# Optimization experiments

Measured on AMD Instinct MI355X. Metric: run time of the kernel, lower is better.

Reference implementation:

```python
import jax, jax.numpy as jnp
import numpy as np

CHEB_K = 3

def avwgcn(x, E, w_pool, b_pool):
    # x: [B,N,C], E: [N,D], w_pool: [D,K,C,O], b_pool: [D,O]
    N = E.shape[0]
    supports = jax.nn.softmax(jax.nn.relu(E @ E.T), axis=1)  # [N,N]
    slist = [jnp.eye(N, dtype=x.dtype), supports]
    for _ in range(CHEB_K - 2):
        slist.append(2.0 * supports @ slist[-1] - slist[-2])
    S = jnp.stack(slist)                         # [K,N,N]
    W = jnp.einsum('nd,dkio->nkio', E, w_pool)   # [N,K,C,O]
    b = E @ b_pool                               # [N,O]
    xg = jnp.einsum('knm,bmc->bnkc', S, x)       # [B,N,K,C]
    return jnp.einsum('bnki,nkio->bno', xg, W) + b


def setup_inputs() -> dict:
    key = jax.random.key(0)
    ks = jax.random.split(key, 9)
    B, N, C_IN, C_OUT, D = 16, 2048, 64, 64, 10
    x = jax.random.normal(ks[0], (B, N, C_IN), dtype=jnp.float32)
    state = jax.random.normal(ks[1], (B, N, C_OUT), dtype=jnp.float32)
    node_embeddings = jax.random.normal(ks[2], (N, D), dtype=jnp.float32)
    gate_wpool = jax.random.normal(ks[3], (D, CHEB_K, C_IN + C_OUT, 2 * C_OUT), dtype=jnp.float32) * 0.1
    gate_bpool = jax.random.normal(ks[4], (D, 2 * C_OUT), dtype=jnp.float32) * 0.1
    upd_wpool = jax.random.normal(ks[5], (D, CHEB_K, C_IN + C_OUT, C_OUT), dtype=jnp.float32) * 0.1
    upd_bpool = jax.random.normal(ks[6], (D, C_OUT), dtype=jnp.float32) * 0.1
    lin_w = jax.random.normal(ks[7], (64, 128), dtype=jnp.float32) * 0.1
    lin_b = jax.random.normal(ks[8], (64,), dtype=jnp.float32) * 0.1
    return {"x": x, "state": state, "node_embeddings": node_embeddings,
            "gate_wpool": gate_wpool, "gate_bpool": gate_bpool,
            "upd_wpool": upd_wpool, "upd_bpool": upd_bpool,
            "lin_w": lin_w, "lin_b": lin_b}


def reference(x, state, node_embeddings, gate_wpool, gate_bpool, upd_wpool, upd_bpool, lin_w, lin_b):
    input_and_state = jnp.concatenate([x, state], axis=-1)          # [B,N,128]
    z_r = jax.nn.sigmoid(avwgcn(input_and_state, node_embeddings, gate_wpool, gate_bpool))  # [B,N,128]
    z_r = z_r @ lin_w.T + lin_b                                     # [B,N,64]
    candidate = jnp.concatenate([x, z_r], axis=-1)                  # [B,N,128]
    hc = jnp.tanh(avwgcn(candidate, node_embeddings, upd_wpool, upd_bpool))  # [B,N,64]
    return hc
```

## Files before the change

### kernel.cpp

```cpp
#include <hip/hip_runtime.h>

typedef unsigned short u16;
typedef short s16x8 __attribute__((ext_vector_type(8)));
typedef _Float16 h16x8 __attribute__((ext_vector_type(8)));
typedef float f32x4 __attribute__((ext_vector_type(4)));
typedef u16 u16x4 __attribute__((ext_vector_type(4)));

#define DEV static __device__ __forceinline__

DEV u16 f2h(float x){ union { _Float16 h; u16 u; } v; v.h = (_Float16)x; return v.u; }
DEV float h2f(u16 u){ union { u16 u; _Float16 h; } v; v.u = u; return (float)v.h; }
DEV void split_h(float x, u16& h, u16& l){
    h = f2h(x);
    l = f2h(x - h2f(h));
}
DEV h16x8 H8(s16x8 v){ union { s16x8 s; h16x8 h; } u; u.s = v; return u.h; }
DEV f32x4 mfma16(s16x8 a, s16x8 b, f32x4 c){
    return __builtin_amdgcn_mfma_f32_16x16x32_f16(H8(a), H8(b), c, 0, 0, 0);
}

DEV int swz(int r, int m){ return (m & ~0x38) | ((((m >> 3) ^ r) & 7) << 3); }

DEV void gll16(const u16* g, u16* l){
    __builtin_amdgcn_global_load_lds((const __attribute__((address_space(1))) void*)g,
                                     (__attribute__((address_space(3))) void*)l, 16, 0, 0);
}

__global__ __launch_bounds__(256) void k_prep(const float* __restrict__ E,
    const float* __restrict__ gwp, const float* __restrict__ gbp,
    const float* __restrict__ uwp, const float* __restrict__ ubp,
    const float* __restrict__ lw,
    u16* __restrict__ wg, u16* __restrict__ wu,
    float* __restrict__ bg, float* __restrict__ bu,
    u16* __restrict__ lwt,
    u16* __restrict__ Sh, u16* __restrict__ Sl)
{
    __shared__ float red[8];
    const int tid = threadIdx.x;
    if (blockIdx.x < 2048){
        const int n = blockIdx.x;
        const int w = tid >> 6, lane = tid & 63;
        float en[10];
        #pragma unroll
        for (int d = 0; d < 10; d++) en[d] = E[n*10 + d];
        float v[8];
        #pragma unroll
        for (int i = 0; i < 8; i++){
            int m = tid + i*256;
            const float* em = E + m*10;
            float s = 0.f;
            #pragma unroll
            for (int d = 0; d < 10; d++) s += en[d]*em[d];
            v[i] = fmaxf(s, 0.f);
        }
        float mx = v[0];
        #pragma unroll
        for (int i = 1; i < 8; i++) mx = fmaxf(mx, v[i]);
        #pragma unroll
        for (int off = 32; off > 0; off >>= 1) mx = fmaxf(mx, __shfl_xor(mx, off));
        if (lane == 0) red[w] = mx;
        __syncthreads();
        mx = fmaxf(fmaxf(red[0], red[1]), fmaxf(red[2], red[3]));
        __syncthreads();
        float sum = 0.f;
        #pragma unroll
        for (int i = 0; i < 8; i++){ v[i] = __expf(v[i] - mx); sum += v[i]; }
        #pragma unroll
        for (int off = 32; off > 0; off >>= 1) sum += __shfl_xor(sum, off);
        if (lane == 0) red[4 + w] = sum;
        __syncthreads();
        sum = red[4] + red[5] + red[6] + red[7];
        float inv = 1.f / sum;
        #pragma unroll
        for (int i = 0; i < 8; i++){
            float p = v[i] * inv;
            u16 h, l; split_h(p, h, l);
            int ms = swz(n, tid + i*256);
            Sh[n*2048 + ms] = h;
            Sl[n*2048 + ms] = l;
        }
        return;
    }
    long idx = (long)(blockIdx.x - 2048)*256 + tid;
    if (idx < 491520){
        int kk = (int)(idx & 31);
        int o  = (int)((idx >> 5) & 127);
        int r2 = (int)(idx >> 12);
        int d = r2 % 10, jc = r2 / 10;
        int j = jc*32 + kk;
        int k = j >> 7, i = j & 127;
        float v = gwp[(((d*3 + k)*128) + i)*128 + o];
        wg[idx] = f2h(v);
    } else if (idx < 737280){
        long t = idx - 491520;
        int kk = (int)(t & 31);
        int o  = (int)((t >> 5) & 63);
        int r2 = (int)(t >> 11);
        int d = r2 % 10, jc = r2 / 10;
        int j = jc*32 + kk;
        int k = j >> 7, i = j & 127;
        float v = uwp[(((d*3 + k)*128) + i)*64 + o];
        wu[t] = f2h(v);
    } else if (idx < 999424){
        long t = idx - 737280; int n = (int)(t >> 7), o = (int)(t & 127);
        float s = 0.f;
        #pragma unroll
        for (int d = 0; d < 10; d++) s += E[n*10+d]*gbp[d*128+o];
        bg[t] = s;
    } else if (idx < 1130496){
        long t = idx - 999424; int n = (int)(t >> 6), o = (int)(t & 63);
        float s = 0.f;
        #pragma unroll
        for (int d = 0; d < 10; d++) s += E[n*10+d]*ubp[d*64+o];
        bu[t] = s;
    } else if (idx < 1138688){
        long t = idx - 1130496;
        lwt[t] = f2h(lw[t]);
    }
}

__global__ __launch_bounds__(256) void k_packx(const float* __restrict__ x,
                                               const float* __restrict__ state,
                                               u16* __restrict__ xt)
{
    __shared__ u16 T[64*264];
    const int tid = threadIdx.x;
    const int ct = blockIdx.x & 31;
    const int mt = blockIdx.x >> 5;
    const int colG0 = ct << 6;
    const int m0 = mt << 8;
    const int b = colG0 >> 7, c0 = colG0 & 127;
    const float* src = (c0 < 64) ? (x + ((long)b*2048 + m0)*64)
                                 : (state + ((long)b*2048 + m0)*64);
    #pragma unroll
    for (int p = 0; p < 16; p++){
        int m = p*16 + (tid >> 4);
        int c4 = (tid & 15) << 2;
        f32x4 v = *(const f32x4*)(src + (long)m*64 + c4);
        #pragma unroll
        for (int q = 0; q < 4; q++)
            T[(c4 + q)*264 + m] = f2h(v[q]);
    }
    __syncthreads();
    #pragma unroll
    for (int p = 0; p < 8; p++){
        int cg = (tid >> 5) + p*8;
        int colG = colG0 + cg;
        int mc = (tid & 31) << 3;
        s16x8 val = *(const s16x8*)&T[cg*264 + mc];
        int ms = swz(colG, m0 + mc);
        *(s16x8*)(xt + (long)colG*2048 + ms) = val;
    }
}

template<int EPI>
__global__ __launch_bounds__(256) void k_gemm(
    const u16* __restrict__ Ah, const u16* __restrict__ Al,
    const u16* __restrict__ Bt,
    u16* __restrict__ Ot, float* __restrict__ Orow,
    const u16* __restrict__ Xt)
{
    __shared__ __attribute__((aligned(16))) u16 AsH[2][64*64];
    __shared__ __attribute__((aligned(16))) u16 AsL[2][64*64];
    __shared__ __attribute__((aligned(16))) u16 Bs[2][128*64];
    const int tid = threadIdx.x;
    const int xc = blockIdx.x & 7, ii = blockIdx.x >> 3;
    const int bm = ((xc & 3)*8 + (ii & 7)) << 6;
    const int bn = ((xc >> 2)*8 + (ii >> 3)) << 7;
    const int w = tid >> 6, lane = tid & 63;
    const int wm = (w & 1) << 5;
    const int wn = (w >> 1) << 6;
    const int lr = lane & 15, lk = lane >> 4;

    const int srow = tid >> 3, scol = (tid & 7) << 3;
    const long a0 = (long)(bm + srow)*2048 + scol;
    const long a1 = a0 + 32*2048;
    const long b0 = (long)(bn + srow)*2048 + scol;
    const long b1 = b0 + 32*2048;
    const long b2 = b0 + 64*2048;
    const long b3 = b0 + 96*2048;
    const int l0 = tid*8, l1 = tid*8 + 2048;

    const int c0 = (lk ^ (lr & 7)) << 3;
    const int c1 = c0 ^ 32;

#define STAGE(B, K) do { \
        gll16(Ah + a0 + (K), &AsH[B][l0]); \
        gll16(Ah + a1 + (K), &AsH[B][l1]); \
        gll16(Al + a0 + (K), &AsL[B][l0]); \
        gll16(Al + a1 + (K), &AsL[B][l1]); \
        gll16(Bt + b0 + (K), &Bs[B][l0]); \
        gll16(Bt + b1 + (K), &Bs[B][l1]); \
        gll16(Bt + b2 + (K), &Bs[B][l0 + 4096]); \
        gll16(Bt + b3 + (K), &Bs[B][l1 + 4096]); \
    } while(0)

    f32x4 acc[2][4];
    const f32x4 Z4 = {0.f, 0.f, 0.f, 0.f};
    #pragma unroll
    for (int i = 0; i < 2; i++)
        #pragma unroll
        for (int j = 0; j < 4; j++) acc[i][j] = Z4;

    STAGE(0, 0);
    __syncthreads();
    int cur = 0;
    for (int k0 = 0; k0 < 2048; k0 += 64){
        if (k0 + 64 < 2048) STAGE(cur ^ 1, k0 + 64);
        const u16* ah = AsH[cur];
        const u16* al = AsL[cur];
        const u16* bs = Bs[cur];
        #pragma unroll
        for (int s2 = 0; s2 < 2; s2++){
            const int cc = s2 ? c1 : c0;
            s16x8 bfv[4], af[2];
            #pragma unroll
            for (int ni = 0; ni < 4; ni++)
                bfv[ni] = *(const s16x8*)&bs[(wn + ni*16 + lr)*64 + cc];
            #pragma unroll
            for (int mi = 0; mi < 2; mi++)
                af[mi] = *(const s16x8*)&ah[(wm + mi*16 + lr)*64 + cc];
            #pragma unroll
            for (int mi = 0; mi < 2; mi++)
                #pragma unroll
                for (int ni = 0; ni < 4; ni++)
                    acc[mi][ni] = mfma16(af[mi], bfv[ni], acc[mi][ni]);
            #pragma unroll
            for (int mi = 0; mi < 2; mi++)
                af[mi] = *(const s16x8*)&al[(wm + mi*16 + lr)*64 + cc];
            #pragma unroll
            for (int mi = 0; mi < 2; mi++)
                #pragma unroll
                for (int ni = 0; ni < 4; ni++)
                    acc[mi][ni] = mfma16(af[mi], bfv[ni], acc[mi][ni]);
        }
        __syncthreads();
        cur ^= 1;
    }
#undef STAGE

    #pragma unroll
    for (int mi = 0; mi < 2; mi++){
        #pragma unroll
        for (int ni = 0; ni < 4; ni++){
            int i0 = bm + wm + mi*16 + lk*4;
            int j  = bn + wn + ni*16 + lr;
            f32x4 v = acc[mi][ni];
            if constexpr (EPI){
                u16x4 xh = *(const u16x4*)(Xt + (long)j*2048 + swz(j, i0));
                #pragma unroll
                for (int r = 0; r < 4; r++)
                    v[r] = 2.f*v[r] - h2f(xh[r]);
            }
            int bb = j >> 7, cc = j & 127;
            float* rp = Orow + ((long)bb*2048 + i0)*128 + cc;
            #pragma unroll
            for (int r = 0; r < 4; r++) rp[(long)r*128] = v[r];
            if constexpr (!EPI){
                u16x4 oh;
                #pragma unroll
                for (int r = 0; r < 4; r++) oh[r] = f2h(v[r]);
                *(u16x4*)(Ot + (long)j*2048 + swz(j, i0)) = oh;
            }
        }
    }
}

__global__ __launch_bounds__(512) void k_combineG(
    const float* __restrict__ G1r, const float* __restrict__ G2r,
    const float* __restrict__ x, const float* __restrict__ second,
    const u16* __restrict__ W,
    const float* __restrict__ bias, const float* __restrict__ E,
    float* __restrict__ out, u16* __restrict__ XtT,
    const u16* __restrict__ lwt, const float* __restrict__ lb)
{
    __shared__ u16 Ash[64*40], Asl[64*40];
    __shared__ float Et[640];
    __shared__ u16 Zh[64*136], Zl[64*136];
    const int tid = threadIdx.x, bid = blockIdx.x;
    const int b = bid >> 5, n0 = (bid & 31) << 6;
    const int w = tid >> 6, lane = tid & 63;
    const int wo = w << 4;
    const int lr = lane & 15, lk = lane >> 4;

    for (int i = tid; i < 640; i += 512)
        Et[i] = E[(n0 + (i & 63))*10 + (i >> 6)];

    const f32x4 Z4 = {0.f, 0.f, 0.f, 0.f};
    f32x4 acc[4];
    #pragma unroll
    for (int mi = 0; mi < 4; mi++) acc[mi] = Z4;

    const long rowbase = (long)b*2048 + n0;
    const int laneoff = (wo + lr)*32 + lk*8;

    s16x8 pbh[3];

    for (int jc = 0; jc < 12; jc++){
        {
            const long t0 = (long)(jc*10 + 0)*128*32;
            const long t1 = (long)(jc*10 + 1)*128*32;
            pbh[0] = *(const s16x8*)(W + t0 + laneoff);
            pbh[1] = *(const s16x8*)(W + t1 + laneoff);
        }
        __syncthreads();
        {
            const float* src; int stride;
            if (jc < 4){
                int col0 = jc*32;
                src = (col0 < 64) ? (x + rowbase*64 + col0)
                                  : (second + rowbase*64 + (col0 - 64));
                stride = 64;
            } else if (jc < 8){
                src = G1r + rowbase*128 + (jc-4)*32; stride = 128;
            } else {
                src = G2r + rowbase*128 + (jc-8)*32; stride = 128;
            }
            int row = tid >> 3, c4 = (tid & 7)*4;
            f32x4 s0 = *(const f32x4*)(src + (long)row*stride + c4);
            u16x4 vh, vl;
            #pragma unroll
            for (int t = 0; t < 4; t++){
                u16 h,l; split_h(s0[t], h, l); vh[t]=h; vl[t]=l;
            }
            *(u16x4*)&Ash[row*40 + c4] = vh;
            *(u16x4*)&Asl[row*40 + c4] = vl;
        }
        __syncthreads();

        s16x8 ah[4], al[4];
        #pragma unroll
        for (int mi = 0; mi < 4; mi++){
            ah[mi] = *(const s16x8*)&Ash[(mi*16 + lr)*40 + lk*8];
            al[mi] = *(const s16x8*)&Asl[(mi*16 + lr)*40 + lk*8];
        }

        #pragma unroll
        for (int d = 0; d < 10; d++){
            const int cur = d % 3;
            if (d < 8){
                const int nx = (d + 2) % 3;
                const long t2 = (long)(jc*10 + d + 2)*128*32;
                pbh[nx] = *(const s16x8*)(W + t2 + laneoff);
            }
            f32x4 Cd[4];
            __builtin_amdgcn_s_setprio(1);
            #pragma unroll
            for (int mi = 0; mi < 4; mi++)
                Cd[mi] = mfma16(ah[mi], pbh[cur], Z4);
            #pragma unroll
            for (int mi = 0; mi < 4; mi++)
                Cd[mi] = mfma16(al[mi], pbh[cur], Cd[mi]);
            __builtin_amdgcn_s_setprio(0);
            #pragma unroll
            for (int mi = 0; mi < 4; mi++){
                f32x4 e4 = *(const f32x4*)&Et[d*64 + mi*16 + lk*4];
                acc[mi] += e4 * Cd[mi];
            }
        }
    }

    #pragma unroll
    for (int mi = 0; mi < 4; mi++){
        int lrow = mi*16 + lk*4;
        int o = wo + lr;
        #pragma unroll
        for (int r = 0; r < 4; r++){
            float v = acc[mi][r] + bias[(long)(n0 + lrow + r)*128 + o];
            v = 1.f/(1.f + __expf(-v));
            u16 h, l; split_h(v, h, l);
            Zh[(lrow + r)*136 + o] = h;
            Zl[(lrow + r)*136 + o] = l;
        }
    }
    __syncthreads();
    f32x4 az[2] = {Z4, Z4};
    const int ow = (w & 3) << 4;
    const int rh = (w >> 2) << 5;
    #pragma unroll
    for (int ks = 0; ks < 4; ks++){
        s16x8 bw = *(const s16x8*)(lwt + (ow + lr)*128 + ks*32 + lk*8);
        #pragma unroll
        for (int mi = 0; mi < 2; mi++){
            s16x8 zh = *(const s16x8*)&Zh[(rh + mi*16 + lr)*136 + ks*32 + lk*8];
            az[mi] = mfma16(zh, bw, az[mi]);
        }
        #pragma unroll
        for (int mi = 0; mi < 2; mi++){
            s16x8 zl = *(const s16x8*)&Zl[(rh + mi*16 + lr)*136 + ks*32 + lk*8];
            az[mi] = mfma16(zl, bw, az[mi]);
        }
    }
    const float lbv = lb[ow + lr];
    const int colG = b*128 + 64 + ow + lr;
    #pragma unroll
    for (int mi = 0; mi < 2; mi++){
        int mrow = n0 + rh + mi*16 + lk*4;
        u16x4 tq;
        #pragma unroll
        for (int r = 0; r < 4; r++){
            float v = az[mi][r] + lbv;
            out[((long)b*2048 + mrow + r)*64 + ow + lr] = v;
            tq[r] = f2h(v);
        }
        *(u16x4*)(XtT + (long)colG*2048 + swz(colG, mrow)) = tq;
    }
}

__global__ __launch_bounds__(512) void k_combineU(
    const float* __restrict__ G1r, const float* __restrict__ G2r,
    const float* __restrict__ x, const float* __restrict__ second,
    const u16* __restrict__ W,
    const float* __restrict__ bias, const float* __restrict__ E,
    float* __restrict__ out)
{
    __shared__ u16 Ash[64*40], Asl[64*40];
    __shared__ float Et[640];
    const int tid = threadIdx.x, bid = blockIdx.x;
    const int b = bid >> 5, n0 = (bid & 31) << 6;
    const int w = tid >> 6, lane = tid & 63;
    const int ow = (w & 3) << 4;
    const int rh = (w >> 2) << 5;
    const int lr = lane & 15, lk = lane >> 4;

    for (int i = tid; i < 640; i += 512)
        Et[i] = E[(n0 + (i & 63))*10 + (i >> 6)];

    const f32x4 Z4 = {0.f, 0.f, 0.f, 0.f};
    f32x4 acc[2];
    #pragma unroll
    for (int mi = 0; mi < 2; mi++) acc[mi] = Z4;

    const long rowbase = (long)b*2048 + n0;
    const int laneoff = (ow + lr)*32 + lk*8;

    s16x8 pbh[3];

    for (int jc = 0; jc < 12; jc++){
        {
            const long t0 = (long)(jc*10 + 0)*64*32;
            const long t1 = (long)(jc*10 + 1)*64*32;
            pbh[0] = *(const s16x8*)(W + t0 + laneoff);
            pbh[1] = *(const s16x8*)(W + t1 + laneoff);
        }
        __syncthreads();
        {
            const float* src; int stride;
            if (jc < 4){
                int col0 = jc*32;
                src = (col0 < 64) ? (x + rowbase*64 + col0)
                                  : (second + rowbase*64 + (col0 - 64));
                stride = 64;
            } else if (jc < 8){
                src = G1r + rowbase*128 + (jc-4)*32; stride = 128;
            } else {
                src = G2r + rowbase*128 + (jc-8)*32; stride = 128;
            }
            int row = tid >> 3, c4 = (tid & 7)*4;
            f32x4 s0 = *(const f32x4*)(src + (long)row*stride + c4);
            u16x4 vh, vl;
            #pragma unroll
            for (int t = 0; t < 4; t++){
                u16 h,l; split_h(s0[t], h, l); vh[t]=h; vl[t]=l;
            }
            *(u16x4*)&Ash[row*40 + c4] = vh;
            *(u16x4*)&Asl[row*40 + c4] = vl;
        }
        __syncthreads();

        s16x8 ah[2], al[2];
        #pragma unroll
        for (int mi = 0; mi < 2; mi++){
            ah[mi] = *(const s16x8*)&Ash[(rh + mi*16 + lr)*40 + lk*8];
            al[mi] = *(const s16x8*)&Asl[(rh + mi*16 + lr)*40 + lk*8];
        }

        #pragma unroll
        for (int d = 0; d < 10; d++){
            const int cur = d % 3;
            if (d < 8){
                const int nx = (d + 2) % 3;
                const long t2 = (long)(jc*10 + d + 2)*64*32;
                pbh[nx] = *(const s16x8*)(W + t2 + laneoff);
            }
            f32x4 Cd[2];
            __builtin_amdgcn_s_setprio(1);
            #pragma unroll
            for (int mi = 0; mi < 2; mi++)
                Cd[mi] = mfma16(ah[mi], pbh[cur], Z4);
            #pragma unroll
            for (int mi = 0; mi < 2; mi++)
                Cd[mi] = mfma16(al[mi], pbh[cur], Cd[mi]);
            __builtin_amdgcn_s_setprio(0);
            #pragma unroll
            for (int mi = 0; mi < 2; mi++){
                f32x4 e4 = *(const f32x4*)&Et[d*64 + rh + mi*16 + lk*4];
                acc[mi] += e4 * Cd[mi];
            }
        }
    }

    #pragma unroll
    for (int mi = 0; mi < 2; mi++){
        int mrow = n0 + rh + mi*16 + lk*4;
        int o = ow + lr;
        #pragma unroll
        for (int r = 0; r < 4; r++){
            float v = acc[mi][r] + bias[(long)(mrow + r)*64 + o];
            v = tanhf(v);
            out[((long)b*2048 + mrow + r)*64 + o] = v;
        }
    }
}

extern "C" void kernel_launch(void* const* d_in, const int* in_sizes, int n_in,
                              void* d_out, int out_size, void* d_ws, size_t ws_size,
                              hipStream_t stream)
{
    const float* x   = (const float*)d_in[0];
    const float* st  = (const float*)d_in[1];
    const float* E   = (const float*)d_in[2];
    const float* gwp = (const float*)d_in[3];
    const float* gbp = (const float*)d_in[4];
    const float* uwp = (const float*)d_in[5];
    const float* ubp = (const float*)d_in[6];
    const float* lw  = (const float*)d_in[7];
    const float* lb  = (const float*)d_in[8];
    float* out = (float*)d_out;
    char* ws = (char*)d_ws;

    const size_t MB8 = 8388608;
    u16*   Sh   = (u16*)(ws);
    u16*   Sl   = (u16*)(ws + 1*MB8);
    u16*   Xt   = (u16*)(ws + 2*MB8);
    u16*   G1t  = (u16*)(ws + 3*MB8);
    float* G1row= (float*)(ws + 4*MB8);
    float* G2row= (float*)(ws + 6*MB8);
    float* zr   = (float*)(ws + 8*MB8);
    char*  p    = ws + 9*MB8;
    u16* wg = (u16*)p;             p += 983040;
    u16* wu = (u16*)p;             p += 491520;
    float* bg = (float*)p;         p += 1048576;
    float* bu = (float*)p;         p += 524288;
    u16* lwt = (u16*)p;            p += 16384;

    k_prep<<<dim3(6497), dim3(256), 0, stream>>>(E, gwp, gbp, uwp, ubp, lw,
                                                 wg, wu, bg, bu, lwt, Sh, Sl);
    k_packx<<<dim3(256), dim3(256), 0, stream>>>(x, st, Xt);
    k_gemm<0><<<dim3(512), dim3(256), 0, stream>>>(Sh, Sl, Xt, G1t, G1row,
                                                   (const u16*)nullptr);
    k_gemm<1><<<dim3(512), dim3(256), 0, stream>>>(Sh, Sl, G1t, (u16*)nullptr, G2row,
                                                   Xt);
    k_combineG<<<dim3(512), dim3(512), 0, stream>>>(G1row, G2row, x, st,
                                                    wg, bg, E, zr, Xt, lwt, lb);
    k_gemm<0><<<dim3(512), dim3(256), 0, stream>>>(Sh, Sl, Xt, G1t, G1row,
                                                   (const u16*)nullptr);
    k_gemm<1><<<dim3(512), dim3(256), 0, stream>>>(Sh, Sl, G1t, (u16*)nullptr, G2row,
                                                   Xt);
    k_combineU<<<dim3(512), dim3(512), 0, stream>>>(G1row, G2row, x, zr,
                                                    wu, bu, E, out);
}
```

Baseline: 354.8 us.

## Reuse first-layer graph products for x columns; propagate only z_r in second layer

The second AVWGCN's graph diffusion now runs only on the 64 new z_r channels per batch. The S·x and S²·x parts (the x half of the input) are reused from the first layer's GEMM outputs instead of being recomputed. The second pair of GEMMs therefore covers half the columns with half the grid. combineU reads its K-stage inputs from the two sets of buffers. This costs extra workspace and a smaller second GEMM grid that may underfill the GPU.

```diff
diff --git a/kernel.cpp b/kernel.cpp
--- a/kernel.cpp
+++ b/kernel.cpp
@@ -153,20 +153,22 @@
     }
 }
 
-template<int EPI>
+template<int EPI, int NCT>
 __global__ __launch_bounds__(256) void k_gemm(
     const u16* __restrict__ Ah, const u16* __restrict__ Al,
     const u16* __restrict__ Bt,
     u16* __restrict__ Ot, float* __restrict__ Orow,
     const u16* __restrict__ Xt)
 {
+    constexpr int COLS = NCT*8;
+    constexpr int CSH  = (NCT == 16) ? 7 : 6;
     __shared__ __attribute__((aligned(16))) u16 AsH[2][64*64];
     __shared__ __attribute__((aligned(16))) u16 AsL[2][64*64];
     __shared__ __attribute__((aligned(16))) u16 Bs[2][128*64];
     const int tid = threadIdx.x;
     const int xc = blockIdx.x & 7, ii = blockIdx.x >> 3;
     const int bm = ((xc & 3)*8 + (ii & 7)) << 6;
-    const int bn = ((xc >> 2)*8 + (ii >> 3)) << 7;
+    const int bn = ((xc >> 2)*(NCT/2) + (ii >> 3)) << 7;
     const int w = tid >> 6, lane = tid & 63;
     const int wm = (w & 1) << 5;
     const int wn = (w >> 1) << 6;
@@ -252,10 +254,10 @@
                 for (int r = 0; r < 4; r++)
                     v[r] = 2.f*v[r] - h2f(xh[r]);
             }
-            int bb = j >> 7, cc = j & 127;
-            float* rp = Orow + ((long)bb*2048 + i0)*128 + cc;
-            #pragma unroll
-            for (int r = 0; r < 4; r++) rp[(long)r*128] = v[r];
+            int bb = j >> CSH, cc = j & (COLS-1);
+            float* rp = Orow + ((long)bb*2048 + i0)*COLS + cc;
+            #pragma unroll
+            for (int r = 0; r < 4; r++) rp[(long)r*COLS] = v[r];
             if constexpr (!EPI){
                 u16x4 oh;
                 #pragma unroll
@@ -271,7 +273,7 @@
     const float* __restrict__ x, const float* __restrict__ second,
     const u16* __restrict__ W,
     const float* __restrict__ bias, const float* __restrict__ E,
-    float* __restrict__ out, u16* __restrict__ XtT,
+    float* __restrict__ out, u16* __restrict__ Zt,
     const u16* __restrict__ lwt, const float* __restrict__ lb)
 {
     __shared__ u16 Ash[64*40], Asl[64*40];
@@ -392,7 +394,7 @@
         }
     }
     const float lbv = lb[ow + lr];
-    const int colG = b*128 + 64 + ow + lr;
+    const int colZ = b*64 + ow + lr;
     #pragma unroll
     for (int mi = 0; mi < 2; mi++){
         int mrow = n0 + rh + mi*16 + lk*4;
@@ -403,13 +405,14 @@
             out[((long)b*2048 + mrow + r)*64 + ow + lr] = v;
             tq[r] = f2h(v);
         }
-        *(u16x4*)(XtT + (long)colG*2048 + swz(colG, mrow)) = tq;
+        *(u16x4*)(Zt + (long)colZ*2048 + swz(colZ, mrow)) = tq;
     }
 }
 
 __global__ __launch_bounds__(512) void k_combineU(
     const float* __restrict__ G1r, const float* __restrict__ G2r,
-    const float* __restrict__ x, const float* __restrict__ second,
+    const float* __restrict__ G1z, const float* __restrict__ G2z,
+    const float* __restrict__ x, const float* __restrict__ zr,
     const u16* __restrict__ W,
     const float* __restrict__ bias, const float* __restrict__ E,
     float* __restrict__ out)
@@ -446,15 +449,13 @@
         __syncthreads();
         {
             const float* src; int stride;
-            if (jc < 4){
-                int col0 = jc*32;
-                src = (col0 < 64) ? (x + rowbase*64 + col0)
-                                  : (second + rowbase*64 + (col0 - 64));
-                stride = 64;
-            } else if (jc < 8){
-                src = G1r + rowbase*128 + (jc-4)*32; stride = 128;
-            } else {
-                src = G2r + rowbase*128 + (jc-8)*32; stride = 128;
+            switch (jc >> 1){
+                case 0: src = x   + rowbase*64  + (jc&1)*32;  stride = 64;  break;
+                case 1: src = zr  + rowbase*64  + (jc&1)*32;  stride = 64;  break;
+                case 2: src = G1r + rowbase*128 + (jc&1)*32;  stride = 128; break;
+                case 3: src = G1z + rowbase*64  + (jc&1)*32;  stride = 64;  break;
+                case 4: src = G2r + rowbase*128 + (jc&1)*32;  stride = 128; break;
+                default:src = G2z + rowbase*64  + (jc&1)*32;  stride = 64;  break;
             }
             int row = tid >> 3, c4 = (tid & 7)*4;
             f32x4 s0 = *(const f32x4*)(src + (long)row*stride + c4);
@@ -529,15 +530,19 @@
     float* out = (float*)d_out;
     char* ws = (char*)d_ws;
 
-    const size_t MB8 = 8388608;
+    const size_t MB4 = 4194304;
     u16*   Sh   = (u16*)(ws);
-    u16*   Sl   = (u16*)(ws + 1*MB8);
-    u16*   Xt   = (u16*)(ws + 2*MB8);
-    u16*   G1t  = (u16*)(ws + 3*MB8);
-    float* G1row= (float*)(ws + 4*MB8);
-    float* G2row= (float*)(ws + 6*MB8);
-    float* zr   = (float*)(ws + 8*MB8);
-    char*  p    = ws + 9*MB8;
+    u16*   Sl   = (u16*)(ws + 2*MB4);
+    u16*   Xt   = (u16*)(ws + 4*MB4);
+    u16*   G1t  = (u16*)(ws + 6*MB4);
+    float* G1row= (float*)(ws + 8*MB4);
+    float* G2row= (float*)(ws + 12*MB4);
+    float* zr   = (float*)(ws + 16*MB4);
+    u16*   Zt   = (u16*)(ws + 18*MB4);
+    u16*   G1zt = (u16*)(ws + 19*MB4);
+    float* G1z  = (float*)(ws + 20*MB4);
+    float* G2z  = (float*)(ws + 22*MB4);
+    char*  p    = ws + 24*MB4;
     u16* wg = (u16*)p;             p += 983040;
     u16* wu = (u16*)p;             p += 491520;
     float* bg = (float*)p;         p += 1048576;
@@ -547,16 +552,16 @@
     k_prep<<<dim3(6497), dim3(256), 0, stream>>>(E, gwp, gbp, uwp, ubp, lw,
                                                  wg, wu, bg, bu, lwt, Sh, Sl);
     k_packx<<<dim3(256), dim3(256), 0, stream>>>(x, st, Xt);
-    k_gemm<0><<<dim3(512), dim3(256), 0, stream>>>(Sh, Sl, Xt, G1t, G1row,
-                                                   (const u16*)nullptr);
-    k_gemm<1><<<dim3(512), dim3(256), 0, stream>>>(Sh, Sl, G1t, (u16*)nullptr, G2row,
-                                                   Xt);
+    k_gemm<0,16><<<dim3(512), dim3(256), 0, stream>>>(Sh, Sl, Xt, G1t, G1row,
+                                                      (const u16*)nullptr);
+    k_gemm<1,16><<<dim3(512), dim3(256), 0, stream>>>(Sh, Sl, G1t, (u16*)nullptr,
+                                                      G2row, Xt);
     k_combineG<<<dim3(512), dim3(512), 0, stream>>>(G1row, G2row, x, st,
-                                                    wg, bg, E, zr, Xt, lwt, lb);
-    k_gemm<0><<<dim3(512), dim3(256), 0, stream>>>(Sh, Sl, Xt, G1t, G1row,
-                                                   (const u16*)nullptr);
-    k_gemm<1><<<dim3(512), dim3(256), 0, stream>>>(Sh, Sl, G1t, (u16*)nullptr, G2row,
-                                                   Xt);
-    k_combineU<<<dim3(512), dim3(512), 0, stream>>>(G1row, G2row, x, zr,
-                                                    wu, bu, E, out);
-}
+                                                    wg, bg, E, zr, Zt, lwt, lb);
+    k_gemm<0,8><<<dim3(256), dim3(256), 0, stream>>>(Sh, Sl, Zt, G1zt, G1z,
+                                                     (const u16*)nullptr);
+    k_gemm<1,8><<<dim3(256), dim3(256), 0, stream>>>(Sh, Sl, G1zt, (u16*)nullptr,
+                                                     G2z, Zt);
+    k_combineU<<<dim3(512), dim3(512), 0, stream>>>(G1row, G2row, G1z, G2z,
+                                                    x, zr, wu, bu, E, out);
+}
```

Measured after the change: 337.3 us. -4.9%, faster.
